# Optimization experiments

Hardware: AMD Instinct MI355X
Metric: run time of the kernel (lower is better)

The kernel has to match this reference:

```python
import jax, jax.numpy as jnp
import numpy as np

# pywt db4 decomposition lowpass filter
DEC_LO = np.array([-0.010597401785069032, 0.0328830116668852, 0.030841381835560764,
                   -0.18703481171909309, -0.027983769416859854, 0.6308807679298589,
                   0.7148465705529157, 0.2303778133088965])
# pytorch_wavelets pre-reverses filters so that torch's cross-correlation conv1d
# implements true convolution; lax.conv_general_dilated is also cross-correlation,
# so we use the same reversed kernel.
KERNEL_LO = jnp.asarray(DEC_LO[::-1].copy(), dtype=jnp.float32)
FLEN = 8


def dwt_lo(x):
    # Single-level db4 lowpass analysis with 'zero' padding, matching
    # pytorch_wavelets afb1d (mode='zero'). x: [B, N, D] -> [B, (N+7)//2, D]
    B, N, D = x.shape
    out = (N + FLEN - 1) // 2            # pywt.dwt_coeff_len(N, 8, 'zero')
    p = 2 * (out - 1) - N + FLEN         # total zero padding
    xr = x.transpose(0, 2, 1).reshape(B * D, 1, N)
    y = jax.lax.conv_general_dilated(xr, KERNEL_LO[None, None, :],
                                     window_strides=(2,),
                                     padding=[(p // 2, p - p // 2)])
    return y.reshape(B, D, out).transpose(0, 2, 1)


def setup_inputs() -> dict:
    key = jax.random.key(0)
    k1, k2 = jax.random.split(key)
    x = jax.random.normal(k1, (32, 4097, 768), dtype=jnp.float32)
    cls_attention_map = jax.random.uniform(k2, (32, 4096), dtype=jnp.float32)
    return {"x": x, "cls_attention_map": cls_attention_map}


def reference(x, cls_attention_map):
    factors = jnp.array([1.5, 0.5], dtype=jnp.float32)  # sorted descending
    B, N, D = x.shape
    cls_tok, patches = x[:, :1], x[:, 1:]

    # per-sample entropy of the CLS attention map
    ent = -jnp.sum(cls_attention_map * jnp.log2(cls_attention_map + 1e-9), axis=-1)  # [B]
    mean, std = ent.mean(), ent.std(ddof=1)  # torch .std() is unbiased
    thr = mean - factors * std               # [2]
    lvl = jnp.sum(ent[:, None] < thr[None, :], axis=1)          # [B]
    lvl = jnp.where(std < 1e-6, jnp.ones_like(lvl), lvl)        # degenerate-std fallback
    lvl = jnp.clip(lvl, 1, factors.shape[0])                    # clamp_min_(1)

    # compute both experts densely, then per-sample select (replaces gather/scatter)
    y1 = dwt_lo(patches)   # level-1 Yl : [B, L1, D], L1 = 2051
    y2 = dwt_lo(y1)        # level-2 Yl : [B, L2, D], L2 = 1029 (cascaded lowpass = J=2 cA)
    L1, L2 = y1.shape[1], y2.shape[1]
    y2p = jnp.pad(y2, ((0, 0), (0, L1 - L2), (0, 0)))

    is1 = (lvl == 1)
    final_patches = jnp.where(is1[:, None, None], y1, y2p)      # [B, L1, D]
    out_len = jnp.where(is1, L1, L2)                            # [B]

    final_x = jnp.concatenate([cls_tok, final_patches], axis=1)  # [B, 1+L1, D]
    mask = jnp.arange(L1)[None, :] < out_len[:, None]
    mask = jnp.concatenate([jnp.ones((B, 1), dtype=bool), mask], axis=1)
    return final_x, mask
```

## Files before the change

kernel.cpp:

```cpp
#include <hip/hip_runtime.h>
#include <hip/hip_bf16.h>
#include <math.h>


#define B_       32
#define NTOK     4097
#define NPATCH   4096
#define D_       768
#define L1_      2051
#define L2_      1029
#define OUTROWS  2052
#define TOUT     16

__device__ __constant__ float KLO[8] = {
     0.2303778133088965f,
     0.7148465705529157f,
     0.6308807679298589f,
    -0.027983769416859854f,
    -0.18703481171909309f,
     0.030841381835560764f,
     0.0328830116668852f,
    -0.010597401785069032f
};

__device__ __forceinline__ float dot8(const float w[8]) {
    float v = KLO[0] * w[0];
    v = fmaf(KLO[1], w[1], v);
    v = fmaf(KLO[2], w[2], v);
    v = fmaf(KLO[3], w[3], v);
    v = fmaf(KLO[4], w[4], v);
    v = fmaf(KLO[5], w[5], v);
    v = fmaf(KLO[6], w[6], v);
    v = fmaf(KLO[7], w[7], v);
    return v;
}

__global__ void ent_kernel(const float* __restrict__ att, double* __restrict__ ent) {
    __shared__ double sm[256];
    const int b = blockIdx.x;
    const float* a = att + (size_t)b * NPATCH;
    double acc = 0.0;
    for (int i = threadIdx.x; i < NPATCH; i += 256) {
        double v = (double)a[i];
        acc += v * log2(v + 1e-9);
    }
    sm[threadIdx.x] = acc;
    __syncthreads();
    for (int s = 128; s > 0; s >>= 1) {
        if (threadIdx.x < s) sm[threadIdx.x] += sm[threadIdx.x + s];
        __syncthreads();
    }
    if (threadIdx.x == 0) ent[b] = -sm[0];
}

__global__ void lvl_kernel(const double* __restrict__ ent, int* __restrict__ lvl) {
    if (threadIdx.x == 0 && blockIdx.x == 0) {
        double m = 0.0;
        for (int i = 0; i < B_; ++i) m += ent[i];
        m /= (double)B_;
        double v = 0.0;
        for (int i = 0; i < B_; ++i) { double d = ent[i] - m; v += d * d; }
        v /= (double)(B_ - 1);
        double s = sqrt(v);
        double thr0 = m - 1.5 * s;
        for (int i = 0; i < B_; ++i)
            lvl[i] = (s < 1e-6) ? 1 : ((ent[i] < thr0) ? 2 : 1);
    }
}

__global__ __launch_bounds__(256) void dwt_kernel(const float* __restrict__ x,
                                                  const int* __restrict__ lvl,
                                                  float* __restrict__ out) {
    const int d  = blockIdx.y * 256 + threadIdx.x;
    const int b  = blockIdx.z;
    const int o0 = blockIdx.x * TOUT;
    const int L  = lvl[b];

    const float* xb = x + (size_t)b * NTOK * D_ + d;
    float* ob = out + (size_t)b * OUTROWS * D_ + d;

    if (blockIdx.x == 0) ob[0] = xb[0];

    auto xload = [&](int q) -> float {
        const int n = q - 6;
        return (n >= 0 && n < NPATCH) ? xb[(size_t)(n + 1) * D_] : 0.0f;
    };

    if (L == 1) {
        float xw[8];
        const int q0 = 2 * o0;
#pragma unroll
        for (int t = 0; t < 8; ++t) xw[t] = xload(q0 + t);
#pragma unroll
        for (int s = 0; s < TOUT; ++s) {
            const int o = o0 + s;
            if (o < L1_) ob[(size_t)(o + 1) * D_] = dot8(xw);
#pragma unroll
            for (int t = 0; t < 6; ++t) xw[t] = xw[t + 2];
            xw[6] = xload(q0 + 2 * s + 8);
            xw[7] = xload(q0 + 2 * s + 9);
        }
    } else {
        if (o0 >= L2_) {
#pragma unroll
            for (int s = 0; s < TOUT; ++s) {
                const int o = o0 + s;
                if (o < L1_) ob[(size_t)(o + 1) * D_] = 0.0f;
            }
            return;
        }
        int j = 2 * o0 - 6;
        float xw[8];
#pragma unroll
        for (int t = 0; t < 8; ++t) xw[t] = xload(2 * j + t);

        auto produce = [&]() -> float {
            float v = 0.0f;
            if (j >= 0 && j < L1_) v = dot8(xw);
#pragma unroll
            for (int t = 0; t < 6; ++t) xw[t] = xw[t + 2];
            xw[6] = xload(2 * j + 8);
            xw[7] = xload(2 * j + 9);
            ++j;
            return v;
        };

        float yw[8];
#pragma unroll
        for (int t = 0; t < 8; ++t) yw[t] = produce();
#pragma unroll
        for (int s = 0; s < TOUT; ++s) {
            const int o = o0 + s;
            if (o < L1_) {
                float v = (o < L2_) ? dot8(yw) : 0.0f;
                ob[(size_t)(o + 1) * D_] = v;
            }
#pragma unroll
            for (int t = 0; t < 6; ++t) yw[t] = yw[t + 2];
            yw[6] = produce();
            yw[7] = produce();
        }
    }
}

__global__ void mask_kernel(const int* __restrict__ lvl, float* __restrict__ mask) {
    const int idx = blockIdx.x * 256 + threadIdx.x;
    if (idx >= B_ * OUTROWS) return;
    const int b = idx / OUTROWS;
    const int j = idx % OUTROWS;
    const int len = (lvl[b] == 1) ? L1_ : L2_;
    mask[idx] = (j == 0 || (j - 1) < len) ? 1.0f : 0.0f;
}

extern "C" void kernel_launch(void* const* d_in, const int* in_sizes, int n_in,
                              void* d_out, int out_size, void* d_ws, size_t ws_size,
                              hipStream_t stream) {
    const float* x   = (const float*)d_in[0];
    const float* att = (const float*)d_in[1];
    float* out  = (float*)d_out;
    float* mask = out + (size_t)B_ * OUTROWS * D_;

    double* ent = (double*)d_ws;
    int*    lvl = (int*)((char*)d_ws + B_ * sizeof(double));

    ent_kernel<<<B_, 256, 0, stream>>>(att, ent);
    lvl_kernel<<<1, 64, 0, stream>>>(ent, lvl);

    dim3 grid((L1_ + TOUT - 1) / TOUT, D_ / 256, B_);
    dwt_kernel<<<grid, 256, 0, stream>>>(x, lvl, out);

    mask_kernel<<<(B_ * OUTROWS + 255) / 256, 256, 0, stream>>>(lvl, mask);
}
```

Before: 139.8 us.

## Vectorize DWT kernel to float4, fuse mask write, use nontemporal stores

Each thread now processes four adjacent channels with float4 loads and stores. A block covers all 768 channels of a batch row tile with 192 threads, and the separate mask kernel is folded into the DWT kernel. Output stores use nontemporal hints so they bypass cache retention. This cuts the number of memory instructions and removes one launch. The cost is four times the register pressure from the f4 sliding windows.

```diff
diff --git a/kernel.cpp b/kernel.cpp
--- a/kernel.cpp
+++ b/kernel.cpp
@@ -3,10 +3,13 @@
 #include <math.h>
 
 
+typedef float f4 __attribute__((ext_vector_type(4)));
+
 #define B_       32
 #define NTOK     4097
 #define NPATCH   4096
 #define D_       768
+#define D4_      192
 #define L1_      2051
 #define L2_      1029
 #define OUTROWS  2052
@@ -23,16 +26,16 @@
     -0.010597401785069032f
 };
 
-__device__ __forceinline__ float dot8(const float w[8]) {
-    float v = KLO[0] * w[0];
-    v = fmaf(KLO[1], w[1], v);
-    v = fmaf(KLO[2], w[2], v);
-    v = fmaf(KLO[3], w[3], v);
-    v = fmaf(KLO[4], w[4], v);
-    v = fmaf(KLO[5], w[5], v);
-    v = fmaf(KLO[6], w[6], v);
-    v = fmaf(KLO[7], w[7], v);
-    return v;
+__device__ __forceinline__ f4 dot8v(const f4 w[8]) {
+    f4 a = KLO[0] * w[0];
+#pragma unroll
+    for (int t = 1; t < 8; ++t) {
+        a.x = fmaf(KLO[t], w[t].x, a.x);
+        a.y = fmaf(KLO[t], w[t].y, a.y);
+        a.z = fmaf(KLO[t], w[t].z, a.z);
+        a.w = fmaf(KLO[t], w[t].w, a.w);
+    }
+    return a;
 }
 
 __global__ void ent_kernel(const float* __restrict__ att, double* __restrict__ ent) {
@@ -68,33 +71,44 @@
     }
 }
 
-__global__ __launch_bounds__(256) void dwt_kernel(const float* __restrict__ x,
+__global__ __launch_bounds__(192) void dwt_kernel(const f4* __restrict__ x,
                                                   const int* __restrict__ lvl,
-                                                  float* __restrict__ out) {
-    const int d  = blockIdx.y * 256 + threadIdx.x;
-    const int b  = blockIdx.z;
+                                                  f4* __restrict__ out,
+                                                  float* __restrict__ mask) {
+    const int d  = threadIdx.x;
+    const int b  = blockIdx.y;
     const int o0 = blockIdx.x * TOUT;
     const int L  = lvl[b];
 
-    const float* xb = x + (size_t)b * NTOK * D_ + d;
-    float* ob = out + (size_t)b * OUTROWS * D_ + d;
+    const f4* xb = x + (size_t)b * NTOK * D4_ + d;
+    f4* ob = out + (size_t)b * OUTROWS * D4_ + d;
 
     if (blockIdx.x == 0) ob[0] = xb[0];
 
-    auto xload = [&](int q) -> float {
+    {
+        const int len = (L == 1) ? L1_ : L2_;
+        const int o = o0 + d;
+        if (d < TOUT && o < L1_)
+            mask[(size_t)b * OUTROWS + o + 1] = (o < len) ? 1.0f : 0.0f;
+        if (blockIdx.x == 0 && d == TOUT)
+            mask[(size_t)b * OUTROWS] = 1.0f;
+    }
+
+    const f4 z4 = (f4)(0.0f);
+    auto xload = [&](int q) -> f4 {
         const int n = q - 6;
-        return (n >= 0 && n < NPATCH) ? xb[(size_t)(n + 1) * D_] : 0.0f;
+        return (n >= 0 && n < NPATCH) ? xb[(size_t)(n + 1) * D4_] : z4;
     };
 
     if (L == 1) {
-        float xw[8];
+        f4 xw[8];
         const int q0 = 2 * o0;
 #pragma unroll
         for (int t = 0; t < 8; ++t) xw[t] = xload(q0 + t);
 #pragma unroll
         for (int s = 0; s < TOUT; ++s) {
             const int o = o0 + s;
-            if (o < L1_) ob[(size_t)(o + 1) * D_] = dot8(xw);
+            if (o < L1_) __builtin_nontemporal_store(dot8v(xw), &ob[(size_t)(o + 1) * D4_]);
 #pragma unroll
             for (int t = 0; t < 6; ++t) xw[t] = xw[t + 2];
             xw[6] = xload(q0 + 2 * s + 8);
@@ -105,18 +119,18 @@
 #pragma unroll
             for (int s = 0; s < TOUT; ++s) {
                 const int o = o0 + s;
-                if (o < L1_) ob[(size_t)(o + 1) * D_] = 0.0f;
+                if (o < L1_) __builtin_nontemporal_store(z4, &ob[(size_t)(o + 1) * D4_]);
             }
             return;
         }
         int j = 2 * o0 - 6;
-        float xw[8];
+        f4 xw[8];
 #pragma unroll
         for (int t = 0; t < 8; ++t) xw[t] = xload(2 * j + t);
 
-        auto produce = [&]() -> float {
-            float v = 0.0f;
-            if (j >= 0 && j < L1_) v = dot8(xw);
+        auto produce = [&]() -> f4 {
+            f4 v = z4;
+            if (j >= 0 && j < L1_) v = dot8v(xw);
 #pragma unroll
             for (int t = 0; t < 6; ++t) xw[t] = xw[t + 2];
             xw[6] = xload(2 * j + 8);
@@ -125,15 +139,15 @@
             return v;
         };
 
-        float yw[8];
+        f4 yw[8];
 #pragma unroll
         for (int t = 0; t < 8; ++t) yw[t] = produce();
 #pragma unroll
         for (int s = 0; s < TOUT; ++s) {
             const int o = o0 + s;
             if (o < L1_) {
-                float v = (o < L2_) ? dot8(yw) : 0.0f;
-                ob[(size_t)(o + 1) * D_] = v;
+                f4 v = (o < L2_) ? dot8v(yw) : z4;
+                __builtin_nontemporal_store(v, &ob[(size_t)(o + 1) * D4_]);
             }
 #pragma unroll
             for (int t = 0; t < 6; ++t) yw[t] = yw[t + 2];
@@ -141,15 +155,6 @@
             yw[7] = produce();
         }
     }
-}
-
-__global__ void mask_kernel(const int* __restrict__ lvl, float* __restrict__ mask) {
-    const int idx = blockIdx.x * 256 + threadIdx.x;
-    if (idx >= B_ * OUTROWS) return;
-    const int b = idx / OUTROWS;
-    const int j = idx % OUTROWS;
-    const int len = (lvl[b] == 1) ? L1_ : L2_;
-    mask[idx] = (j == 0 || (j - 1) < len) ? 1.0f : 0.0f;
 }
 
 extern "C" void kernel_launch(void* const* d_in, const int* in_sizes, int n_in,
@@ -166,8 +171,6 @@
     ent_kernel<<<B_, 256, 0, stream>>>(att, ent);
     lvl_kernel<<<1, 64, 0, stream>>>(ent, lvl);
 
-    dim3 grid((L1_ + TOUT - 1) / TOUT, D_ / 256, B_);
-    dwt_kernel<<<grid, 256, 0, stream>>>(x, lvl, out);
-
-    mask_kernel<<<(B_ * OUTROWS + 255) / 256, 256, 0, stream>>>(lvl, mask);
+    dim3 grid((L1_ + TOUT - 1) / TOUT, B_, 1);
+    dwt_kernel<<<grid, 192, 0, stream>>>((const f4*)x, lvl, (f4*)out, mask);
 }
```

Result: faster. 130.9 us (-6.4%).
